# Performance work log

Hardware: AMD Instinct MI355X
Metric: run time of the kernel (lower is better)

## Reference

```python
import jax, jax.numpy as jnp
import numpy as np
import math

EMBED_DIM = 1024
NUM_HEADS = 16
HEAD_DIM = EMBED_DIM // NUM_HEADS
BLOCK_SIZE = 64
NUM_RAND_BLOCKS = 3
B, L = 2, 2048


def _build_sparse_mask(seq_len, block_size, num_rand_blocks, seed=0):
    """BigBird block-sparse mask: global (first/last block) + window (prev/self/next) + random blocks."""
    nb = seq_len // block_size
    bm = np.zeros((nb, nb), dtype=bool)
    # global: first and last blocks attend to all / are attended by all
    bm[0, :] = True
    bm[:, 0] = True
    bm[-1, :] = True
    bm[:, -1] = True
    # sliding window for interior blocks
    for b in range(1, nb - 1):
        bm[b, max(b - 1, 0):b + 2] = True
    # random blocks for interior blocks (deterministic for reproducibility)
    rng = np.random.default_rng(seed)
    for b in range(1, nb - 1):
        avail = [x for x in range(nb) if x != b]
        picks = rng.permutation(len(avail))[:num_rand_blocks]
        for p in picks:
            bm[b, avail[p]] = True
    # expand block mask to token-level [L, L]
    return np.kron(bm, np.ones((block_size, block_size), dtype=bool))


def setup_inputs() -> dict:
    key = jax.random.key(0)
    k0, k1, k2, k3, k4 = jax.random.split(key, 5)
    hidden_states = jax.random.normal(k0, (B, L, EMBED_DIM), dtype=jnp.float32)
    s = 0.02
    # torch nn.Linear weights have shape [out_features, in_features]
    Wq = jax.random.normal(k1, (EMBED_DIM, EMBED_DIM), dtype=jnp.float32) * s
    Wk = jax.random.normal(k2, (EMBED_DIM, EMBED_DIM), dtype=jnp.float32) * s
    Wv = jax.random.normal(k3, (EMBED_DIM, EMBED_DIM), dtype=jnp.float32) * s
    Wo = jax.random.normal(k4, (EMBED_DIM, EMBED_DIM), dtype=jnp.float32) * s
    sparse_mask = jnp.asarray(_build_sparse_mask(L, BLOCK_SIZE, NUM_RAND_BLOCKS))
    return {"hidden_states": hidden_states, "Wq": Wq, "Wk": Wk, "Wv": Wv,
            "Wo": Wo, "sparse_mask": sparse_mask}


def reference(hidden_states, Wq, Wk, Wv, Wo, sparse_mask):
    Bsz, Lq, D = hidden_states.shape
    H, hd = NUM_HEADS, HEAD_DIM
    # projections (Linear no bias): x @ W.T
    q = (hidden_states @ Wq.T).reshape(Bsz, Lq, H, hd).transpose(0, 2, 1, 3)
    k = (hidden_states @ Wk.T).reshape(Bsz, Lq, H, hd).transpose(0, 2, 1, 3)
    v = (hidden_states @ Wv.T).reshape(Bsz, Lq, H, hd).transpose(0, 2, 1, 3)
    # dense scores with block-sparse mask (matches reference module's math)
    scores = jnp.einsum('bhqd,bhkd->bhqk', q, k) / math.sqrt(hd)  # [B,H,L,L]
    scores = jnp.where(sparse_mask[None, None, :, :], scores, -jnp.inf)
    attn = jax.nn.softmax(scores.astype(jnp.float32), axis=-1).astype(scores.dtype)
    out = jnp.einsum('bhqk,bhkd->bhqd', attn, v)
    out = out.transpose(0, 2, 1, 3).reshape(Bsz, Lq, D)
    out = out @ Wo.T
    return out
```

## Files before the change

kernel.cpp:

```cpp
#include <hip/hip_runtime.h>
#include <hip/hip_bf16.h>
#include <stdint.h>

#define LSEQ   2048
#define DMODEL 1024
#define NHEADS 16
#define HDIM   64
#define NB     32
#define BATCH  2
#define NGRP   38
#define NWG_ATTN (32 * NGRP)

typedef unsigned short u16;
typedef __attribute__((ext_vector_type(8))) __bf16 bf16x8;
typedef __attribute__((ext_vector_type(4))) float f32x4;
typedef __attribute__((ext_vector_type(4))) unsigned int u32x4;
typedef __attribute__((ext_vector_type(4))) u16 u16x4;


__device__ __forceinline__ u16 f2b(float f) {
  unsigned b = __float_as_uint(f);
  return (u16)((b + 0x7FFFu + ((b >> 16) & 1u)) >> 16);
}

__device__ __forceinline__ void lds_dma16(const u16* g, u16* l) {
  __builtin_amdgcn_global_load_lds(
      (__attribute__((address_space(1))) const void*)g,
      (__attribute__((address_space(3))) void*)l, 16, 0, 0);
}

__device__ __forceinline__ bool probe_is_bf16(const void* src) {
  const u16* p = (const u16*)src;
  int cnt = 0;
  #pragma unroll
  for (int i = 0; i < 64; ++i) {
    int e = (p[i] >> 7) & 0xFF;
    cnt += (e >= 100 && e <= 140) ? 1 : 0;
  }
  return cnt >= 48;
}

__device__ __forceinline__ bool mask_block(const void* m, int qb, int kb) {
  const unsigned char* p = (const unsigned char*)m;
  size_t e = (size_t)(qb * 64) * LSEQ + (size_t)kb * 64;
  unsigned char b0 = p[0], b1 = p[1], b2 = p[2];
  if (b0 == 1 && b1 == 1) return p[e] != 0;
  if (b0 == 1 && b1 == 0 && b2 == 1) return ((const u16*)m)[e] != 0;
  if (b0 == 1) return ((const unsigned int*)m)[e] != 0;
  if (b0 == 0x80 && b1 == 0x3f) return ((const u16*)m)[e] != 0;
  return ((const float*)m)[e] != 0.0f;
}

__global__ __launch_bounds__(256) void convert_kernel(
    const void* __restrict__ hs, const void* __restrict__ wq,
    const void* __restrict__ wk, const void* __restrict__ wv,
    const void* __restrict__ wo, u16* __restrict__ dst,
    const void* __restrict__ mask, int* __restrict__ skb,
    f32x4* __restrict__ zbuf, int zn4) {
  __shared__ int sflags;
  if (threadIdx.x == 0)
    sflags = (probe_is_bf16(hs) ? 1 : 0) | (probe_is_bf16(wq) ? 2 : 0);
  __syncthreads();
  bool bf_hs = (sflags & 1) != 0, bf_w = (sflags & 2) != 0;
  if (blockIdx.x == 0 && threadIdx.x < NB) {
    int qb = threadIdx.x;
    int base = (qb == 0) ? 0 : ((qb == 31) ? 32 : (64 + (qb - 1) * 8));
    int cap = (qb == 0 || qb == 31) ? 32 : 8;
    int c = 0;
    for (int kb = 0; kb < NB; ++kb)
      if (mask_block(mask, qb, kb)) skb[base + c++] = kb;
    for (; c < cap; ++c) skb[base + c] = -1;
  }
  const int HS4 = BATCH * LSEQ * DMODEL / 4;
  const int W4 = DMODEL * DMODEL / 4;
  int total4 = HS4 + 4 * W4;
  int stride = gridDim.x * blockDim.x;
  if (!(bf_hs && bf_w)) {
    for (int i = blockIdx.x * blockDim.x + threadIdx.x; i < total4; i += stride) {
      const void* src;
      int off;
      bool isbf;
      if (i < HS4) { src = hs; off = i; isbf = bf_hs; }
      else {
        int j = i - HS4;
        int wsel = j >> 18;
        off = j & (W4 - 1);
        src = (wsel == 0) ? wq : (wsel == 1) ? wk : (wsel == 2) ? wv : wo;
        isbf = bf_w;
      }
      if (isbf) continue;
      f32x4 f = ((const f32x4*)src)[off];
      ((u16x4*)dst)[i] = (u16x4){f2b(f[0]), f2b(f[1]), f2b(f[2]), f2b(f[3])};
    }
  }
  for (int i = blockIdx.x * blockDim.x + threadIdx.x; i < zn4; i += stride)
    zbuf[i] = (f32x4){0.f, 0.f, 0.f, 0.f};
}

#define QBM 256
#define QBN 256
#define QBK 64

#define BAR()  __builtin_amdgcn_s_barrier()
#define LGK0() asm volatile("s_waitcnt lgkmcnt(0)" ::: "memory")
#define VM4()  asm volatile("s_waitcnt vmcnt(4)" ::: "memory")
#define VM0()  asm volatile("s_waitcnt vmcnt(0)" ::: "memory")

#define STG_A(p, h, kt) do { \
    lds_dma16(Abase + ((h)*128 +  0)*1024 + (kt)*64, sA + (p)*16384 + (h)*8192 +        wb8); \
    lds_dma16(Abase + ((h)*128 + 64)*1024 + (kt)*64, sA + (p)*16384 + (h)*8192 + 4096 + wb8); \
  } while (0)
#define STG_B(p, h, kt) do { \
    lds_dma16(Bbase + ((h)*128 +  0)*1024 + (kt)*64, sB + (p)*16384 + (h)*8192 +        wb8); \
    lds_dma16(Bbase + ((h)*128 + 64)*1024 + (kt)*64, sB + (p)*16384 + (h)*8192 + 4096 + wb8); \
  } while (0)

#define LDA(p, mh) do { \
    const u16* _ba = sA + (p)*16384 + (wr*128 + (mh)*64 + lc)*64; \
    af[0][0] = *(const bf16x8*)(_ba +        x0); af[0][1] = *(const bf16x8*)(_ba +        x1); \
    af[1][0] = *(const bf16x8*)(_ba + 1024 + x0); af[1][1] = *(const bf16x8*)(_ba + 1024 + x1); \
    af[2][0] = *(const bf16x8*)(_ba + 2048 + x0); af[2][1] = *(const bf16x8*)(_ba + 2048 + x1); \
    af[3][0] = *(const bf16x8*)(_ba + 3072 + x0); af[3][1] = *(const bf16x8*)(_ba + 3072 + x1); \
  } while (0)
#define LDB(p, nh) do { \
    const u16* _bb = sB + (p)*16384 + (wc*64 + (nh)*32 + lc)*64; \
    bfr[nh][0][0] = *(const bf16x8*)(_bb +        x0); bfr[nh][0][1] = *(const bf16x8*)(_bb +        x1); \
    bfr[nh][1][0] = *(const bf16x8*)(_bb + 1024 + x0); bfr[nh][1][1] = *(const bf16x8*)(_bb + 1024 + x1); \
  } while (0)

#define MMQ(mh, nh) do { \
    __builtin_amdgcn_s_setprio(1); \
    _Pragma("unroll") \
    for (int _m = 0; _m < 4; ++_m) { \
      _Pragma("unroll") \
      for (int _n = 0; _n < 2; ++_n) { \
        f32x4 _c = acc[(mh)*4+_m][(nh)*2+_n]; \
        _c = __builtin_amdgcn_mfma_f32_16x16x32_bf16(af[_m][0], bfr[nh][_n][0], _c, 0, 0, 0); \
        _c = __builtin_amdgcn_mfma_f32_16x16x32_bf16(af[_m][1], bfr[nh][_n][1], _c, 0, 0, 0); \
        acc[(mh)*4+_m][(nh)*2+_n] = _c; \
      } \
    } \
    __builtin_amdgcn_s_setprio(0); \
  } while (0)

__global__ __launch_bounds__(512, 2) void gemm_qkv(
    const void* __restrict__ hs_raw, const u16* __restrict__ hs_cv,
    const void* __restrict__ wq_r, const void* __restrict__ wk_r,
    const void* __restrict__ wv_r, const u16* __restrict__ wqb_cv,
    u16* __restrict__ C, u16* __restrict__ C2) {
  extern __shared__ u16 smem[];
  u16* sA = smem;
  u16* sB = smem + 2 * 16384;

  const int t = threadIdx.x;
  const int l = t & 63;
  const int w = t >> 6;
  const int wr = w >> 2;
  const int wc = w & 3;
  const int q4 = l >> 4, lc = l & 15;
  const int tileM = blockIdx.x * QBM;
  const int tileN = blockIdx.y * QBN;
  const int sr = t >> 3;
  const int scs = (((t & 7) ^ ((t >> 3) & 7)) * 8);
  const int wb8 = w * 512;
  const int x0 = (q4 ^ (lc & 7)) * 8;
  const int x1 = x0 ^ 32;

  const bool a_bf = probe_is_bf16(hs_raw);
  const bool b_bf = probe_is_bf16(wq_r);
  const u16* Asrc = a_bf ? (const u16*)hs_raw : hs_cv;
  const int wsel = tileN >> 10;
  const void* wraw = (wsel == 0) ? wq_r : (wsel == 1) ? wk_r : wv_r;
  const u16* Bsrc = b_bf ? (const u16*)wraw + (size_t)(tileN & 1023) * 1024
                         : wqb_cv + (size_t)tileN * 1024;

  const u16* Abase = Asrc + (size_t)(tileM + sr) * 1024 + scs;
  const u16* Bbase = Bsrc + (size_t)sr * 1024 + scs;

  f32x4 acc[8][4] = {};
  bf16x8 af[4][2];
  bf16x8 bfr[2][2][2];

  STG_B(0, 0, 0); STG_B(0, 1, 0);
  STG_A(0, 0, 0); STG_A(0, 1, 0);
  STG_B(1, 0, 1); STG_B(1, 1, 1);
  VM4(); BAR();

  #pragma unroll 1
  for (int j = 0; j < 7; ++j) {
    const int kt0 = 2 * j, kt1 = 2 * j + 1;
    LDA(0, 0); LDB(0, 0); STG_A(1, 0, kt1);
    BAR(); LGK0(); MMQ(0, 0); BAR();
    LDB(0, 1); STG_A(1, 1, kt1);
    BAR(); LGK0(); MMQ(0, 1); BAR();
    LDA(0, 1); STG_B(0, 0, kt0 + 2);
    BAR(); LGK0(); MMQ(1, 1); BAR();
    STG_B(0, 1, kt0 + 2);
    VM4(); BAR(); MMQ(1, 0); BAR();
    LDA(1, 0); LDB(1, 0); STG_A(0, 0, kt0 + 2);
    BAR(); LGK0(); MMQ(0, 0); BAR();
    LDB(1, 1); STG_A(0, 1, kt0 + 2);
    BAR(); LGK0(); MMQ(0, 1); BAR();
    LDA(1, 1); STG_B(1, 0, kt1 + 2);
    BAR(); LGK0(); MMQ(1, 1); BAR();
    STG_B(1, 1, kt1 + 2);
    VM4(); BAR(); MMQ(1, 0); BAR();
  }

  LDA(0, 0); LDB(0, 0); STG_A(1, 0, 15);
  BAR(); LGK0(); MMQ(0, 0); BAR();
  LDB(0, 1); STG_A(1, 1, 15);
  BAR(); LGK0(); MMQ(0, 1); BAR();
  LDA(0, 1);
  BAR(); LGK0(); MMQ(1, 1); BAR();
  VM0(); BAR(); MMQ(1, 0); BAR();
  LDA(1, 0); LDB(1, 0);
  BAR(); LGK0(); MMQ(0, 0); BAR();
  LDB(1, 1);
  BAR(); LGK0(); MMQ(0, 1); BAR();
  LDA(1, 1);
  LGK0(); MMQ(1, 1);
  MMQ(1, 0);

  #pragma unroll
  for (int im = 0; im < 8; ++im)
    #pragma unroll
    for (int jn = 0; jn < 4; ++jn) {
      int rowb = tileM + wr * 128 + im * 16 + q4 * 4;
      int col = tileN + wc * 64 + jn * 16 + lc;
      int sel = col >> 10;
      int o = col & 1023;
      int h = o >> 6, d = o & 63;
      int b = rowb >> 11, ll = rowb & 2047;
      if (sel == 2) {
        u16x4 pk = {f2b(acc[im][jn][0]), f2b(acc[im][jn][1]),
                    f2b(acc[im][jn][2]), f2b(acc[im][jn][3])};
        *(u16x4*)(C2 + ((size_t)((b * NHEADS + h) * HDIM + d)) * LSEQ + ll) = pk;
      } else {
        float scl = (sel == 0) ? 0.125f : 1.0f;
        #pragma unroll
        for (int r = 0; r < 4; ++r) {
          size_t idx = (size_t)sel * (size_t)(BATCH * NHEADS * LSEQ * HDIM) +
                       (((size_t)(b * NHEADS + h) * LSEQ) + ll + r) * HDIM + d;
          C[idx] = f2b(acc[im][jn][r] * scl);
        }
      }
    }
}

#define OTK 32

__global__ __launch_bounds__(256) void gemm_out(
    const u16* __restrict__ A, const void* __restrict__ wo_raw,
    const u16* __restrict__ wo_cv, void* __restrict__ C,
    const void* __restrict__ probe_src) {
  __shared__ u16 lA[128 * OTK];
  __shared__ u16 lB[64 * OTK];
  int t = threadIdx.x;
  int w = t >> 6, l = t & 63, q4 = l >> 4, lc = l & 15;
  int lr = l >> 2, lcc = l & 3;
  int tileM = blockIdx.x * 128, tileN = blockIdx.y * 64;
  int wm = (w >> 1) * 64, wn = (w & 1) * 32;
  bool out_bf = probe_is_bf16(probe_src);
  const u16* Bsrc = probe_is_bf16(wo_raw) ? (const u16*)wo_raw : wo_cv;

  f32x4 acc[4][2] = {};

  for (int kt = 0; kt < 1024; kt += OTK) {
    __syncthreads();
    #pragma unroll
    for (int it = 0; it < 2; ++it) {
      int m = w * 2 + it;
      int row = m * 16 + lr;
      lds_dma16(A + (size_t)(tileM + row) * 1024 + kt + lcc * 8, lA + m * 512);
    }
    {
      int row = w * 16 + lr;
      lds_dma16(Bsrc + (size_t)(tileN + row) * 1024 + kt + lcc * 8, lB + w * 512);
    }
    __syncthreads();
    bf16x8 af[4], bf[2];
    #pragma unroll
    for (int i = 0; i < 4; ++i)
      af[i] = *(const bf16x8*)(lA + (wm + i * 16 + lc) * OTK + q4 * 8);
    #pragma unroll
    for (int j = 0; j < 2; ++j)
      bf[j] = *(const bf16x8*)(lB + (wn + j * 16 + lc) * OTK + q4 * 8);
    #pragma unroll
    for (int i = 0; i < 4; ++i)
      #pragma unroll
      for (int j = 0; j < 2; ++j)
        acc[i][j] = __builtin_amdgcn_mfma_f32_16x16x32_bf16(af[i], bf[j], acc[i][j], 0, 0, 0);
  }

  #pragma unroll
  for (int i = 0; i < 4; ++i)
    #pragma unroll
    for (int j = 0; j < 2; ++j) {
      int rowb = tileM + wm + i * 16 + q4 * 4;
      int col = tileN + wn + j * 16 + lc;
      #pragma unroll
      for (int r = 0; r < 4; ++r) {
        float v = acc[i][j][r];
        size_t idx = (size_t)(rowb + r) * 1024 + col;
        if (out_bf) ((u16*)C)[idx] = f2b(v);
        else ((float*)C)[idx] = v;
      }
    }
}

#define LDP 72

__global__ __launch_bounds__(256) void attn_kernel(
    const u16* __restrict__ qb_, const u16* __restrict__ kb_,
    const u16* __restrict__ vt_, const int* __restrict__ skb,
    float* __restrict__ obuf2, float* __restrict__ lbuf2,
    u16* __restrict__ ctx) {
  __shared__ u16 lK[2][64 * 64];
  __shared__ u16 lV[2][64 * 64];
  __shared__ u16 lP[4][16 * LDP];
  int i = blockIdx.x;
  int bh = (i & 7) + ((i >> 3) & 3) * 8;
  int g = i >> 5;
  int qb = (g < 4) ? 0 : ((g < 8) ? 31 : (g - 7));
  int t = threadIdx.x, w = t >> 6, l = t & 63, q4 = l >> 4, lc = l & 15;
  int r0 = t >> 3, r1 = 32 + (t >> 3);
  int scc = ((t & 7) ^ ((t >> 3) & 7)) * 8;
  const int x0 = (q4 ^ (lc & 7)) * 8;
  const int x1 = x0 ^ 32;

  const u16* qp = qb_ + ((size_t)bh * LSEQ + qb * 64 + w * 16 + lc) * HDIM;
  bf16x8 bq0 = *(const bf16x8*)(qp + q4 * 8);
  bf16x8 bq1 = *(const bf16x8*)(qp + 32 + q4 * 8);

  const u16* kp = kb_ + (size_t)bh * LSEQ * HDIM;
  const u16* vp = vt_ + (size_t)bh * HDIM * LSEQ;
  u16* myP = &lP[w][0];

  f32x4 oacc[4];
  #pragma unroll
  for (int d = 0; d < 4; ++d) oacc[d] = (f32x4){0.f, 0.f, 0.f, 0.f};
  float lp = 0.0f;

  int nkb = 0;
  #pragma unroll
  for (int j = 0; j < 8; ++j) nkb += (skb[g * 8 + j] >= 0) ? 1 : 0;

  auto STAGE = [&](int it, int buf) {
    int kb = skb[g * 8 + it];
    const u16* kblk = kp + (size_t)kb * 64 * HDIM;
    const u16* vblk = vp + kb * 64;
    u16* dK = &lK[buf][0];
    u16* dV = &lV[buf][0];
    lds_dma16(kblk + r0 * HDIM + scc, dK + w * 512);
    lds_dma16(kblk + r1 * HDIM + scc, dK + 2048 + w * 512);
    lds_dma16(vblk + (size_t)r0 * LSEQ + scc, dV + w * 512);
    lds_dma16(vblk + (size_t)r1 * LSEQ + scc, dV + 2048 + w * 512);
  };

  STAGE(0, 0);
  __syncthreads();

  for (int it = 0; it < nkb; ++it) {
    int buf = it & 1;
    if (it + 1 < nkb) STAGE(it + 1, buf ^ 1);
    const u16* bK = &lK[buf][0];
    const u16* bV = &lV[buf][0];

    f32x4 st[4];
    #pragma unroll
    for (int mt = 0; mt < 4; ++mt) {
      const u16* kr = bK + (mt * 16 + lc) * 64;
      bf16x8 k0 = *(const bf16x8*)(kr + x0);
      bf16x8 k1 = *(const bf16x8*)(kr + x1);
      f32x4 z = (f32x4){0.f, 0.f, 0.f, 0.f};
      z = __builtin_amdgcn_mfma_f32_16x16x32_bf16(k0, bq0, z, 0, 0, 0);
      z = __builtin_amdgcn_mfma_f32_16x16x32_bf16(k1, bq1, z, 0, 0, 0);
      st[mt] = z;
    }

    #pragma unroll
    for (int mt = 0; mt < 4; ++mt) {
      float p0 = __expf(st[mt][0]), p1 = __expf(st[mt][1]);
      float p2 = __expf(st[mt][2]), p3 = __expf(st[mt][3]);
      lp += (p0 + p1) + (p2 + p3);
      u16x4 pk = {f2b(p0), f2b(p1), f2b(p2), f2b(p3)};
      *(u16x4*)(myP + lc * LDP + mt * 16 + q4 * 4) = pk;
    }

    bf16x8 ap0 = *(const bf16x8*)(myP + lc * LDP + q4 * 8);
    bf16x8 ap1 = *(const bf16x8*)(myP + lc * LDP + 32 + q4 * 8);
    #pragma unroll
    for (int dt = 0; dt < 4; ++dt) {
      const u16* vr = bV + (dt * 16 + lc) * 64;
      bf16x8 v0 = *(const bf16x8*)(vr + x0);
      bf16x8 v1 = *(const bf16x8*)(vr + x1);
      oacc[dt] = __builtin_amdgcn_mfma_f32_16x16x32_bf16(ap0, v0, oacc[dt], 0, 0, 0);
      oacc[dt] = __builtin_amdgcn_mfma_f32_16x16x32_bf16(ap1, v1, oacc[dt], 0, 0, 0);
    }

    __syncthreads();
  }

  float ltot = lp;
  ltot += __shfl_xor(ltot, 16);
  ltot += __shfl_xor(ltot, 32);

  if (g >= 8) {
    float inv[4];
    #pragma unroll
    for (int r = 0; r < 4; ++r)
      inv[r] = 1.0f / __shfl(ltot, q4 * 4 + r);
    int b = bh >> 4, h = bh & 15;
    #pragma unroll
    for (int dt = 0; dt < 4; ++dt)
      #pragma unroll
      for (int r = 0; r < 4; ++r) {
        float v = oacc[dt][r] * inv[r];
        int grow = qb * 64 + w * 16 + q4 * 4 + r;
        size_t odx = ((size_t)b * LSEQ + grow) * DMODEL + h * HDIM + dt * 16 + lc;
        ctx[odx] = f2b(v);
      }
  } else {
    int s = (qb == 31) ? 1 : 0;
    if (q4 == 0)
      unsafeAtomicAdd(lbuf2 + ((size_t)bh * 2 + s) * 64 + w * 16 + lc, ltot);
    #pragma unroll
    for (int dt = 0; dt < 4; ++dt)
      #pragma unroll
      for (int r = 0; r < 4; ++r)
        unsafeAtomicAdd(obuf2 + (((size_t)bh * 2 + s) * 64 + w * 16 + q4 * 4 + r) * 64 +
                            dt * 16 + lc, oacc[dt][r]);
  }
}

__global__ __launch_bounds__(256) void normalize2_kernel(
    const float* __restrict__ obuf2, const float* __restrict__ lbuf2,
    u16* __restrict__ ctx) {
  int e4 = blockIdx.x * 256 + threadIdx.x;
  int e = e4 * 4;
  int bh = e >> 13;
  int rem = e & 8191;
  int s = rem >> 12, row = (rem >> 6) & 63, d = rem & 63;
  f32x4 o = *(const f32x4*)(obuf2 + e);
  float linv = 1.0f / lbuf2[(bh * 2 + s) * 64 + row];
  int qb = s ? 31 : 0;
  int b = bh >> 4, h = bh & 15;
  int grow = qb * 64 + row;
  u16x4 pk = {f2b(o[0] * linv), f2b(o[1] * linv), f2b(o[2] * linv), f2b(o[3] * linv)};
  *(u16x4*)(ctx + ((size_t)b * LSEQ + grow) * DMODEL + h * HDIM + d) = pk;
}

extern "C" void kernel_launch(void* const* d_in, const int* in_sizes, int n_in,
                              void* d_out, int out_size, void* d_ws, size_t ws_size,
                              hipStream_t stream) {
  const void* hs = d_in[0];
  const void* wq = d_in[1];
  const void* wk = d_in[2];
  const void* wv = d_in[3];
  const void* wo = d_in[4];
  const void* mask = d_in[5];

  u16* hsb = (u16*)d_ws;
  u16* wqb = hsb + 4 * 1024 * 1024;
  u16* wob = wqb + 3 * 1024 * 1024;
  u16* qbuf = wob + 1024 * 1024;
  u16* kbuf = qbuf + 4 * 1024 * 1024;
  u16* vtb  = kbuf + 4 * 1024 * 1024;
  u16* ctx  = vtb + 4 * 1024 * 1024;
  int* skb  = (int*)(ctx + 4 * 1024 * 1024);
  float* obuf2 = (float*)(skb + 512);
  float* lbuf2 = obuf2 + 32 * 2 * 64 * 64;
  const int ZN4 = (32 * 2 * 64 * 64 + 4096) / 4;

  static bool attr_done = false;
  if (!attr_done) {
    hipFuncSetAttribute((const void*)gemm_qkv,
                        hipFuncAttributeMaxDynamicSharedMemorySize, 131072);
    attr_done = true;
  }

  convert_kernel<<<4096, 256, 0, stream>>>(hs, wq, wk, wv, wo, hsb, mask, skb,
                                           (f32x4*)obuf2, ZN4);

  dim3 gqkv(16, 12);
  gemm_qkv<<<gqkv, 512, 131072, stream>>>(hs, hsb, wq, wk, wv, wqb, qbuf, vtb);

  attn_kernel<<<NWG_ATTN, 256, 0, stream>>>(qbuf, kbuf, vtb, skb, obuf2, lbuf2, ctx);

  normalize2_kernel<<<256, 256, 0, stream>>>(obuf2, lbuf2, ctx);

  dim3 gout(32, 16);
  gemm_out<<<gout, 256, 0, stream>>>(ctx, wo, wob, d_out, hs);
}
```

Before: 199.5 us.

## Shrink QKV GEMM N-tile to 192 to fill all CUs

```diff
diff --git a/kernel.cpp b/kernel.cpp
--- a/kernel.cpp
+++ b/kernel.cpp
@@ -98,22 +98,17 @@
 }
 
 #define QBM 256
-#define QBN 256
-#define QBK 64
+#define QBN 192
 
 #define BAR()  __builtin_amdgcn_s_barrier()
 #define LGK0() asm volatile("s_waitcnt lgkmcnt(0)" ::: "memory")
-#define VM4()  asm volatile("s_waitcnt vmcnt(4)" ::: "memory")
+#define VM3()  asm volatile("s_waitcnt vmcnt(3)" ::: "memory")
 #define VM0()  asm volatile("s_waitcnt vmcnt(0)" ::: "memory")
 
-#define STG_A(p, h, kt) do { \
-    lds_dma16(Abase + ((h)*128 +  0)*1024 + (kt)*64, sA + (p)*16384 + (h)*8192 +        wb8); \
-    lds_dma16(Abase + ((h)*128 + 64)*1024 + (kt)*64, sA + (p)*16384 + (h)*8192 + 4096 + wb8); \
-  } while (0)
-#define STG_B(p, h, kt) do { \
-    lds_dma16(Bbase + ((h)*128 +  0)*1024 + (kt)*64, sB + (p)*16384 + (h)*8192 +        wb8); \
-    lds_dma16(Bbase + ((h)*128 + 64)*1024 + (kt)*64, sB + (p)*16384 + (h)*8192 + 4096 + wb8); \
-  } while (0)
+#define STG_A1(p, gi, kt) \
+    lds_dma16(Abase + (gi)*65536 + (kt)*64, sA + (p)*16384 + (gi)*4096 + wb8)
+#define STG_B1(p, Bgp, kt) \
+    lds_dma16((Bgp) + (kt)*64, sB + (p)*12288 + (Bgp##_gi)*4096 + wb8)
 
 #define LDA(p, mh) do { \
     const u16* _ba = sA + (p)*16384 + (wr*128 + (mh)*64 + lc)*64; \
@@ -122,23 +117,19 @@
     af[2][0] = *(const bf16x8*)(_ba + 2048 + x0); af[2][1] = *(const bf16x8*)(_ba + 2048 + x1); \
     af[3][0] = *(const bf16x8*)(_ba + 3072 + x0); af[3][1] = *(const bf16x8*)(_ba + 3072 + x1); \
   } while (0)
-#define LDB(p, nh) do { \
-    const u16* _bb = sB + (p)*16384 + (wc*64 + (nh)*32 + lc)*64; \
-    bfr[nh][0][0] = *(const bf16x8*)(_bb +        x0); bfr[nh][0][1] = *(const bf16x8*)(_bb +        x1); \
-    bfr[nh][1][0] = *(const bf16x8*)(_bb + 1024 + x0); bfr[nh][1][1] = *(const bf16x8*)(_bb + 1024 + x1); \
+#define LDB1(p, nh) do { \
+    const u16* _bb = sB + (p)*12288 + (wc*48 + (nh)*16 + lc)*64; \
+    bfr[nh][0] = *(const bf16x8*)(_bb + x0); bfr[nh][1] = *(const bf16x8*)(_bb + x1); \
   } while (0)
 
-#define MMQ(mh, nh) do { \
+#define MM8(mh, nh) do { \
     __builtin_amdgcn_s_setprio(1); \
     _Pragma("unroll") \
     for (int _m = 0; _m < 4; ++_m) { \
-      _Pragma("unroll") \
-      for (int _n = 0; _n < 2; ++_n) { \
-        f32x4 _c = acc[(mh)*4+_m][(nh)*2+_n]; \
-        _c = __builtin_amdgcn_mfma_f32_16x16x32_bf16(af[_m][0], bfr[nh][_n][0], _c, 0, 0, 0); \
-        _c = __builtin_amdgcn_mfma_f32_16x16x32_bf16(af[_m][1], bfr[nh][_n][1], _c, 0, 0, 0); \
-        acc[(mh)*4+_m][(nh)*2+_n] = _c; \
-      } \
+      f32x4 _c = acc[(mh)*4+_m][nh]; \
+      _c = __builtin_amdgcn_mfma_f32_16x16x32_bf16(af[_m][0], bfr[nh][0], _c, 0, 0, 0); \
+      _c = __builtin_amdgcn_mfma_f32_16x16x32_bf16(af[_m][1], bfr[nh][1], _c, 0, 0, 0); \
+      acc[(mh)*4+_m][nh] = _c; \
     } \
     __builtin_amdgcn_s_setprio(0); \
   } while (0)
@@ -169,65 +160,73 @@
   const bool a_bf = probe_is_bf16(hs_raw);
   const bool b_bf = probe_is_bf16(wq_r);
   const u16* Asrc = a_bf ? (const u16*)hs_raw : hs_cv;
-  const int wsel = tileN >> 10;
-  const void* wraw = (wsel == 0) ? wq_r : (wsel == 1) ? wk_r : wv_r;
-  const u16* Bsrc = b_bf ? (const u16*)wraw + (size_t)(tileN & 1023) * 1024
-                         : wqb_cv + (size_t)tileN * 1024;
-
   const u16* Abase = Asrc + (size_t)(tileM + sr) * 1024 + scs;
-  const u16* Bbase = Bsrc + (size_t)sr * 1024 + scs;
-
-  f32x4 acc[8][4] = {};
+  const u16* Bg0; const u16* Bg1; const u16* Bg2;
+  {
+    int g0 = tileN, g1 = tileN + 64, g2 = tileN + 128;
+    const void* w0 = (g0 >> 10) == 0 ? wq_r : (g0 >> 10) == 1 ? wk_r : wv_r;
+    const void* w1 = (g1 >> 10) == 0 ? wq_r : (g1 >> 10) == 1 ? wk_r : wv_r;
+    const void* w2 = (g2 >> 10) == 0 ? wq_r : (g2 >> 10) == 1 ? wk_r : wv_r;
+    Bg0 = (b_bf ? (const u16*)w0 + (size_t)(g0 & 1023) * 1024
+                : wqb_cv + (size_t)g0 * 1024) + (size_t)sr * 1024 + scs;
+    Bg1 = (b_bf ? (const u16*)w1 + (size_t)(g1 & 1023) * 1024
+                : wqb_cv + (size_t)g1 * 1024) + (size_t)sr * 1024 + scs;
+    Bg2 = (b_bf ? (const u16*)w2 + (size_t)(g2 & 1023) * 1024
+                : wqb_cv + (size_t)g2 * 1024) + (size_t)sr * 1024 + scs;
+  }
+  const int Bg0_gi = 0, Bg1_gi = 1, Bg2_gi = 2;
+
+  f32x4 acc[8][3] = {};
   bf16x8 af[4][2];
-  bf16x8 bfr[2][2][2];
-
-  STG_B(0, 0, 0); STG_B(0, 1, 0);
-  STG_A(0, 0, 0); STG_A(0, 1, 0);
-  STG_B(1, 0, 1); STG_B(1, 1, 1);
-  VM4(); BAR();
+  bf16x8 bfr[3][2];
+
+  STG_B1(0, Bg0, 0); STG_B1(0, Bg1, 0); STG_B1(0, Bg2, 0);
+  STG_A1(0, 0, 0); STG_A1(0, 1, 0); STG_A1(0, 2, 0); STG_A1(0, 3, 0);
+  STG_B1(1, Bg0, 1); STG_B1(1, Bg1, 1); STG_B1(1, Bg2, 1);
+  VM3(); BAR();
 
   #pragma unroll 1
   for (int j = 0; j < 7; ++j) {
-    const int kt0 = 2 * j, kt1 = 2 * j + 1;
-    LDA(0, 0); LDB(0, 0); STG_A(1, 0, kt1);
-    BAR(); LGK0(); MMQ(0, 0); BAR();
-    LDB(0, 1); STG_A(1, 1, kt1);
-    BAR(); LGK0(); MMQ(0, 1); BAR();
-    LDA(0, 1); STG_B(0, 0, kt0 + 2);
-    BAR(); LGK0(); MMQ(1, 1); BAR();
-    STG_B(0, 1, kt0 + 2);
-    VM4(); BAR(); MMQ(1, 0); BAR();
-    LDA(1, 0); LDB(1, 0); STG_A(0, 0, kt0 + 2);
-    BAR(); LGK0(); MMQ(0, 0); BAR();
-    LDB(1, 1); STG_A(0, 1, kt0 + 2);
-    BAR(); LGK0(); MMQ(0, 1); BAR();
-    LDA(1, 1); STG_B(1, 0, kt1 + 2);
-    BAR(); LGK0(); MMQ(1, 1); BAR();
-    STG_B(1, 1, kt1 + 2);
-    VM4(); BAR(); MMQ(1, 0); BAR();
-  }
-
-  LDA(0, 0); LDB(0, 0); STG_A(1, 0, 15);
-  BAR(); LGK0(); MMQ(0, 0); BAR();
-  LDB(0, 1); STG_A(1, 1, 15);
-  BAR(); LGK0(); MMQ(0, 1); BAR();
+    const int kt1 = 2 * j + 1, ktn0 = 2 * j + 2, ktn1 = 2 * j + 3;
+    LDA(0, 0); LDB1(0, 0); LDB1(0, 1); STG_A1(1, 0, kt1); STG_A1(1, 1, kt1);
+    BAR(); LGK0(); MM8(0, 0); MM8(0, 1); BAR();
+    LDB1(0, 2); STG_A1(1, 2, kt1); STG_A1(1, 3, kt1);
+    BAR(); LGK0(); MM8(0, 2); BAR();
+    LDA(0, 1); STG_B1(0, Bg0, ktn0); STG_B1(0, Bg1, ktn0);
+    BAR(); LGK0(); MM8(1, 2); BAR();
+    STG_B1(0, Bg2, ktn0);
+    VM3(); BAR(); MM8(1, 0); MM8(1, 1); BAR();
+    LDA(1, 0); LDB1(1, 0); LDB1(1, 1); STG_A1(0, 0, ktn0); STG_A1(0, 1, ktn0);
+    BAR(); LGK0(); MM8(0, 0); MM8(0, 1); BAR();
+    LDB1(1, 2); STG_A1(0, 2, ktn0); STG_A1(0, 3, ktn0);
+    BAR(); LGK0(); MM8(0, 2); BAR();
+    LDA(1, 1); STG_B1(1, Bg0, ktn1); STG_B1(1, Bg1, ktn1);
+    BAR(); LGK0(); MM8(1, 2); BAR();
+    STG_B1(1, Bg2, ktn1);
+    VM3(); BAR(); MM8(1, 0); MM8(1, 1); BAR();
+  }
+
+  LDA(0, 0); LDB1(0, 0); LDB1(0, 1); STG_A1(1, 0, 15); STG_A1(1, 1, 15);
+  BAR(); LGK0(); MM8(0, 0); MM8(0, 1); BAR();
+  LDB1(0, 2); STG_A1(1, 2, 15); STG_A1(1, 3, 15);
+  BAR(); LGK0(); MM8(0, 2); BAR();
   LDA(0, 1);
-  BAR(); LGK0(); MMQ(1, 1); BAR();
-  VM0(); BAR(); MMQ(1, 0); BAR();
-  LDA(1, 0); LDB(1, 0);
-  BAR(); LGK0(); MMQ(0, 0); BAR();
-  LDB(1, 1);
-  BAR(); LGK0(); MMQ(0, 1); BAR();
+  BAR(); LGK0(); MM8(1, 2); BAR();
+  VM0(); BAR(); MM8(1, 0); MM8(1, 1); BAR();
+  LDA(1, 0); LDB1(1, 0); LDB1(1, 1);
+  BAR(); LGK0(); MM8(0, 0); MM8(0, 1); BAR();
+  LDB1(1, 2);
+  BAR(); LGK0(); MM8(0, 2); BAR();
   LDA(1, 1);
-  LGK0(); MMQ(1, 1);
-  MMQ(1, 0);
+  LGK0(); MM8(1, 2);
+  MM8(1, 0); MM8(1, 1);
 
   #pragma unroll
   for (int im = 0; im < 8; ++im)
     #pragma unroll
-    for (int jn = 0; jn < 4; ++jn) {
+    for (int jn = 0; jn < 3; ++jn) {
       int rowb = tileM + wr * 128 + im * 16 + q4 * 4;
-      int col = tileN + wc * 64 + jn * 16 + lc;
+      int col = tileN + wc * 48 + jn * 16 + lc;
       int sel = col >> 10;
       int o = col & 1023;
       int h = o >> 6, d = o & 63;
@@ -476,15 +475,15 @@
   static bool attr_done = false;
   if (!attr_done) {
     hipFuncSetAttribute((const void*)gemm_qkv,
-                        hipFuncAttributeMaxDynamicSharedMemorySize, 131072);
+                        hipFuncAttributeMaxDynamicSharedMemorySize, 114688);
     attr_done = true;
   }
 
   convert_kernel<<<4096, 256, 0, stream>>>(hs, wq, wk, wv, wo, hsb, mask, skb,
                                            (f32x4*)obuf2, ZN4);
 
-  dim3 gqkv(16, 12);
-  gemm_qkv<<<gqkv, 512, 131072, stream>>>(hs, hsb, wq, wk, wv, wqb, qbuf, vtb);
+  dim3 gqkv(16, 16);
+  gemm_qkv<<<gqkv, 512, 114688, stream>>>(hs, hsb, wq, wk, wv, wqb, qbuf, vtb);
 
   attn_kernel<<<NWG_ATTN, 256, 0, stream>>>(qbuf, kbuf, vtb, skb, obuf2, lbuf2, ctx);
 
```

Measured after the change: 194.3 us. 1.03x faster.
